# Performance work log

Hardware: AMD Instinct MI355X
Metric: run time of the kernel (lower is better)

## Reference

```python
import jax, jax.numpy as jnp
import numpy as np

EPS = 1e-5

def layer_norm(x, gamma):
    mu = jnp.mean(x, axis=-1, keepdims=True)
    var = jnp.mean(jnp.square(x - mu), axis=-1, keepdims=True)
    return (x - mu) / jnp.sqrt(var + EPS) * gamma

def setup_inputs() -> dict:
    key = jax.random.key(0)
    ks = jax.random.split(key, 10)
    b, n, j = 2, 2048, 2048
    dim, ctx_dim, heads, dim_head, ff_mult = 1024, 1024, 16, 64, 4
    inner = heads * dim_head
    ff_inner = ff_mult * dim
    s = 0.02
    return {
        'x': jax.random.normal(ks[0], (b, n, dim), jnp.float32),
        'context': jax.random.normal(ks[1], (b, j, ctx_dim), jnp.float32),
        'mask': jax.random.randint(ks[2], (b, j), 0, 2, jnp.int32),
        'gamma': jnp.ones((dim,), jnp.float32),
        'ctx_gamma': jnp.ones((ctx_dim,), jnp.float32),
        'Wq': jax.random.normal(ks[3], (dim, inner), jnp.float32) * s,
        'Wkv': jax.random.normal(ks[4], (ctx_dim, 2 * dim_head), jnp.float32) * s,
        'Wout': jax.random.normal(ks[5], (inner, dim), jnp.float32) * s,
        'Wff1': jax.random.normal(ks[6], (dim, 2 * ff_inner), jnp.float32) * s,
        'Wff2': jax.random.normal(ks[7], (ff_inner, dim), jnp.float32) * s,
    }

def reference(x, context, mask, gamma, ctx_gamma, Wq, Wkv, Wout, Wff1, Wff2):
    heads, dim_head = 16, 64
    b, n, dim = x.shape
    scale = dim_head ** -0.5
    xn = layer_norm(x, gamma)                              # [b,n,dim]
    ctx = layer_norm(context, ctx_gamma)                   # [b,j,cd]
    q = (xn @ Wq).reshape(b, n, heads, dim_head).transpose(0, 2, 1, 3) * scale  # [b,h,n,d]
    kv = ctx @ Wkv                                         # [b,j,2d]
    k, v = kv[..., :dim_head], kv[..., dim_head:]          # [b,j,d] each (multi-query)
    sim = jnp.einsum('bhid,bjd->bhij', q, k)               # [b,h,n,j]
    sim = jnp.where((mask == 0)[:, None, None, :], -jnp.inf, sim)
    attn = jax.nn.softmax(sim, axis=-1)
    out = jnp.einsum('bhij,bjd->bhid', attn, v)            # [b,h,n,d]
    out = out.transpose(0, 2, 1, 3).reshape(b, n, heads * dim_head)
    out = out @ Wout                                       # [b,n,dim]
    # parallel SwiGLU FF on normalized x
    h = xn @ Wff1
    ff_inner = Wff2.shape[0]
    a, gate = h[..., :ff_inner], h[..., ff_inner:]
    out = out + (jax.nn.silu(gate) * a) @ Wff2
    return out
```

## Files before the change

kernel.cpp:

```cpp
#include <hip/hip_runtime.h>

typedef unsigned short u16;
typedef unsigned int   u32;
typedef __bf16  bf16x8 __attribute__((ext_vector_type(8)));
typedef __bf16  bf16x2 __attribute__((ext_vector_type(2)));
typedef float   f32x4  __attribute__((ext_vector_type(4)));

static __device__ __forceinline__ float b2f(u16 v) {
    return __builtin_bit_cast(float, (u32)(((u32)v) << 16));
}
static __device__ __forceinline__ u16 f2b(float f) {
    u32 u = __builtin_bit_cast(u32, f);
    return (u16)((u + 0x7FFFu + ((u >> 16) & 1u)) >> 16);
}
static __device__ __forceinline__ u32 pack2(float a, float b) {
    bf16x2 t; t[0] = (__bf16)a; t[1] = (__bf16)b;
    return __builtin_bit_cast(u32, t);
}

__global__ __launch_bounds__(256)
void ln_kernel(const float* __restrict__ x, const float* __restrict__ ctx,
               const float* __restrict__ gamma, const float* __restrict__ cgamma,
               u16* __restrict__ xn, u16* __restrict__ ctxn)
{
    const int row = blockIdx.x;
    const int tid = threadIdx.x;
    const float* src; const float* g; u16* dst;
    if (row < 4096) { src = x   + (long)row * 1024;          g = gamma;  dst = xn   + (long)row * 1024; }
    else            { src = ctx + (long)(row - 4096) * 1024; g = cgamma; dst = ctxn + (long)(row - 4096) * 1024; }
    float4 v = ((const float4*)src)[tid];
    float s = v.x + v.y + v.z + v.w;
    float q = v.x*v.x + v.y*v.y + v.z*v.z + v.w*v.w;
#pragma unroll
    for (int off = 32; off; off >>= 1) { s += __shfl_xor(s, off); q += __shfl_xor(q, off); }
    __shared__ float r1[4], r2[4];
    if ((tid & 63) == 0) { r1[tid >> 6] = s; r2[tid >> 6] = q; }
    __syncthreads();
    s = r1[0] + r1[1] + r1[2] + r1[3];
    q = r2[0] + r2[1] + r2[2] + r2[3];
    float mu   = s * (1.0f / 1024.0f);
    float var  = q * (1.0f / 1024.0f) - mu * mu;
    float rstd = rsqrtf(var + 1e-5f);
    float4 gv = ((const float4*)g)[tid];
    ushort4 o;
    o.x = f2b((v.x - mu) * rstd * gv.x);
    o.y = f2b((v.y - mu) * rstd * gv.y);
    o.z = f2b((v.z - mu) * rstd * gv.z);
    o.w = f2b((v.w - mu) * rstd * gv.w);
    ((ushort4*)dst)[tid] = o;
}

__global__ __launch_bounds__(256)
void wconv(const float* __restrict__ W, u16* __restrict__ Wt, int N, int K, float scale)
{
    __shared__ float tile[32][33];
    const int tid = threadIdx.x;
    const int n0 = blockIdx.x * 32;
    const int k0 = blockIdx.y * 32;
    const int r  = tid >> 3;
    const int c4 = (tid & 7) * 4;
    float4 v = *(const float4*)&W[(long)(k0 + r) * N + n0 + c4];
    tile[r][c4 + 0] = v.x; tile[r][c4 + 1] = v.y; tile[r][c4 + 2] = v.z; tile[r][c4 + 3] = v.w;
    __syncthreads();
    ushort4 o;
    o.x = f2b(tile[c4 + 0][r] * scale);
    o.y = f2b(tile[c4 + 1][r] * scale);
    o.z = f2b(tile[c4 + 2][r] * scale);
    o.w = f2b(tile[c4 + 3][r] * scale);
    *(ushort4*)&Wt[(long)(n0 + r) * K + k0 + c4] = o;
}

__global__ __launch_bounds__(256)
void wconv_ff1(const float* __restrict__ W, u16* __restrict__ Wt)
{
    __shared__ float tile[32][33];
    const int tid = threadIdx.x;
    const int a  = blockIdx.x;
    const int k0 = blockIdx.y * 32;
    const int r  = tid >> 3;
    const int c4 = (tid & 7) * 4;
    const int srccol = (c4 < 16) ? (a * 16 + c4) : (4096 + a * 16 + (c4 - 16));
    float4 v = *(const float4*)&W[(long)(k0 + r) * 8192 + srccol];
    tile[r][c4 + 0] = v.x; tile[r][c4 + 1] = v.y; tile[r][c4 + 2] = v.z; tile[r][c4 + 3] = v.w;
    __syncthreads();
    ushort4 o;
    o.x = f2b(tile[c4 + 0][r]);
    o.y = f2b(tile[c4 + 1][r]);
    o.z = f2b(tile[c4 + 2][r]);
    o.w = f2b(tile[c4 + 3][r]);
    *(ushort4*)&Wt[(long)(a * 32 + r) * 1024 + k0 + c4] = o;
}

__global__ __launch_bounds__(256)
void kext_build(const float* __restrict__ kvf, const int* __restrict__ mask,
                u16* __restrict__ kext, float* __restrict__ mbias)
{
    const int gid = blockIdx.x * 256 + threadIdx.x;
    const int b = gid >> 14;
    const int rem = gid & 16383;
    const int j = rem >> 3;
    const int c = rem & 7;
    const float* src = &kvf[((long)b * 2048 + j) * 128 + c * 8];
    u16 ov[8];
#pragma unroll
    for (int e = 0; e < 8; ++e) ov[e] = f2b(src[e]);
    uint4 w;
    w.x = (u32)ov[0] | ((u32)ov[1] << 16);
    w.y = (u32)ov[2] | ((u32)ov[3] << 16);
    w.z = (u32)ov[4] | ((u32)ov[5] << 16);
    w.w = (u32)ov[6] | ((u32)ov[7] << 16);
    *(uint4*)&kext[((long)b * 2048 + j) * 64 + c * 8] = w;
    if (c == 0) mbias[b * 2048 + j] = mask[b * 2048 + j] ? 0.0f : -1e30f;
}

__global__ __launch_bounds__(256)
void vtrans(const float* __restrict__ kvf, u16* __restrict__ vT)
{
    const int j = blockIdx.x * 256 + threadIdx.x;
    const int d = blockIdx.y;
    const int b = blockIdx.z;
    vT[(long)b * 64 * 2048 + (long)d * 2048 + j] =
        f2b(kvf[((long)b * 2048 + j) * 128 + 64 + d]);
}

#define BM 128
#define BN 128
#define BK 32

template<int EPI>
__global__ __launch_bounds__(256, 2)
void gemm_bt(const u16* __restrict__ A, const u16* __restrict__ Bt,
             void* __restrict__ Cv,
             int K, int lda, int ldb, int ldc,
             long aH, long bH, long cH)
{
    __shared__ __align__(16) u16 sm[2][2][BM * BK];
    const int tid  = threadIdx.x;
    const int wave = tid >> 6;
    const int lane = tid & 63;
    const int tn = blockIdx.x * BN;
    const int tm = blockIdx.y * BM;
    const int z  = blockIdx.z;
    A  += (long)z * aH;
    Bt += (long)z * bH;

    const int arow0 = (tid >> 2);
    const int arow1 = 64 + (tid >> 2);
    const int acs0  = (tid & 3) ^ ((arow0 >> 1) & 3);
    const int acs1  = (tid & 3) ^ ((arow1 >> 1) & 3);
    const int nt = K / BK;

#define STAGE(buf, k0)                                                                              \
    do {                                                                                            \
        __builtin_amdgcn_global_load_lds(                                                           \
            (const __attribute__((address_space(1))) void*)(A + (long)(tm + arow0) * lda + (k0) + acs0 * 8),   \
            (__attribute__((address_space(3))) void*)(&sm[buf][0][(wave * 64) * 8]), 16, 0, 0);     \
        __builtin_amdgcn_global_load_lds(                                                           \
            (const __attribute__((address_space(1))) void*)(A + (long)(tm + arow1) * lda + (k0) + acs1 * 8),   \
            (__attribute__((address_space(3))) void*)(&sm[buf][0][(256 + wave * 64) * 8]), 16, 0, 0); \
        __builtin_amdgcn_global_load_lds(                                                           \
            (const __attribute__((address_space(1))) void*)(Bt + (long)(tn + arow0) * ldb + (k0) + acs0 * 8),  \
            (__attribute__((address_space(3))) void*)(&sm[buf][1][(wave * 64) * 8]), 16, 0, 0);     \
        __builtin_amdgcn_global_load_lds(                                                           \
            (const __attribute__((address_space(1))) void*)(Bt + (long)(tn + arow1) * ldb + (k0) + acs1 * 8),  \
            (__attribute__((address_space(3))) void*)(&sm[buf][1][(256 + wave * 64) * 8]), 16, 0, 0); \
    } while (0)

    STAGE(0, 0);

    f32x4 acc[4][4] = {};
    const int wr   = (wave >> 1) * 64;
    const int wc   = (wave & 1) * 64;
    const int frow = lane & 15;
    const int fk   = lane >> 4;

    for (int t = 0; t < nt; ++t) {
        __syncthreads();
        if (t + 1 < nt) STAGE((t + 1) & 1, (t + 1) * BK);
        const int cur = t & 1;
        bf16x8 af[4], bf[4];
#pragma unroll
        for (int m = 0; m < 4; ++m) {
            int row = wr + m * 16 + frow;
            af[m] = *(const bf16x8*)&sm[cur][0][row * BK + ((fk ^ ((row >> 1) & 3)) * 8)];
        }
#pragma unroll
        for (int n = 0; n < 4; ++n) {
            int row = wc + n * 16 + frow;
            bf[n] = *(const bf16x8*)&sm[cur][1][row * BK + ((fk ^ ((row >> 1) & 3)) * 8)];
        }
#pragma unroll
        for (int m = 0; m < 4; ++m)
#pragma unroll
            for (int n = 0; n < 4; ++n)
                acc[m][n] = __builtin_amdgcn_mfma_f32_16x16x32_bf16(af[m], bf[n], acc[m][n], 0, 0, 0);
    }
#undef STAGE

    const long coff = (long)z * cH;
#pragma unroll
    for (int m = 0; m < 4; ++m) {
        const int row0 = tm + wr + m * 16 + fk * 4;
#pragma unroll
        for (int n = 0; n < 4; ++n) {
            const int col = tn + wc + n * 16 + frow;
#pragma unroll
            for (int r = 0; r < 4; ++r) {
                const long off = coff + (long)(row0 + r) * ldc + col;
                const float v = acc[m][n][r];
                if constexpr (EPI == 0)      ((u16*)Cv)[off] = f2b(v);
                else if constexpr (EPI == 1) ((float*)Cv)[off] = v;
                else if constexpr (EPI == 2) ((float*)Cv)[off] += v;
                else                         atomicAdd(&((float*)Cv)[off], v);
            }
        }
    }
}

__global__ __launch_bounds__(512, 2)
void gemm256_ff1(const u16* __restrict__ A, const u16* __restrict__ Bt,
                 u16* __restrict__ C, int K, int lda, int ldb, int ldc)
{
    __shared__ __align__(16) u16 As[2][256 * 64];
    __shared__ __align__(16) u16 Bs[2][256 * 64];
    const int tid  = threadIdx.x;
    const int wave = tid >> 6, lane = tid & 63;
    const int wm = wave >> 2, wn = wave & 3;
    const int frow = lane & 15, fk = lane >> 4;
    const int tn = blockIdx.x * 256;
    const int tm = blockIdx.y * 256;
    const int nt = K >> 6;

    const int lrow  = lane >> 3;
    const int csrc8 = ((lane & 7) ^ lrow) * 8;
    int rbA0[2], rbA1[2], rbB0[2], rbB1[2];
#pragma unroll
    for (int g = 0; g < 2; ++g) {
        const int c = g * 8 + wave;
        const int a0 = ((c >> 3) * 128) + ((c & 7) * 8);
        rbA0[g] = a0; rbA1[g] = a0 + 64;
        const int b0 = ((c >> 2) * 64) + ((c & 3) * 8);
        rbB0[g] = b0; rbB1[g] = b0 + 32;
    }

#define STG(LDS, buf, src, toff, ld, kt, rb)                                                        \
    __builtin_amdgcn_global_load_lds(                                                               \
        (const __attribute__((address_space(1))) void*)((src) + (long)((toff) + (rb) + lrow) * (ld) + ((kt) << 6) + csrc8), \
        (__attribute__((address_space(3))) void*)(&LDS[buf][(rb) * 64]), 16, 0, 0)

#define STAGE_A0(buf, kt) do { STG(As, buf, A,  tm, lda, kt, rbA0[0]); STG(As, buf, A,  tm, lda, kt, rbA0[1]); } while (0)
#define STAGE_A1(buf, kt) do { STG(As, buf, A,  tm, lda, kt, rbA1[0]); STG(As, buf, A,  tm, lda, kt, rbA1[1]); } while (0)
#define STAGE_B0(buf, kt) do { STG(Bs, buf, Bt, tn, ldb, kt, rbB0[0]); STG(Bs, buf, Bt, tn, ldb, kt, rbB0[1]); } while (0)
#define STAGE_B1(buf, kt) do { STG(Bs, buf, Bt, tn, ldb, kt, rbB1[0]); STG(Bs, buf, Bt, tn, ldb, kt, rbB1[1]); } while (0)

    STAGE_B0(0, 0); STAGE_A0(0, 0); STAGE_A1(0, 0); STAGE_B1(0, 0);
    if (nt > 1) {
        STAGE_B0(1, 1); STAGE_A0(1, 1);
        asm volatile("s_waitcnt vmcnt(4)" ::: "memory");
    } else {
        asm volatile("s_waitcnt vmcnt(0)" ::: "memory");
    }
    __builtin_amdgcn_sched_barrier(0);
    __builtin_amdgcn_s_barrier();

    f32x4 acc[8][4] = {};

#define PHASE(mh, nh, STAGE_STMT)                                                                   \
    {                                                                                               \
        bf16x8 af[4][2], bfr[2][2];                                                                 \
        _Pragma("unroll") for (int i = 0; i < 4; ++i) {                                             \
            const int row = wm * 128 + (mh) * 64 + i * 16 + frow;                                   \
            _Pragma("unroll") for (int kk = 0; kk < 2; ++kk)                                        \
                af[i][kk] = *(const bf16x8*)&As[cur][row * 64 + (((kk * 4 + fk) ^ (row & 7)) * 8)]; \
        }                                                                                           \
        _Pragma("unroll") for (int j = 0; j < 2; ++j) {                                             \
            const int row = wn * 64 + (nh) * 32 + j * 16 + frow;                                    \
            _Pragma("unroll") for (int kk = 0; kk < 2; ++kk)                                        \
                bfr[j][kk] = *(const bf16x8*)&Bs[cur][row * 64 + (((kk * 4 + fk) ^ (row & 7)) * 8)];\
        }                                                                                           \
        STAGE_STMT;                                                                                 \
        __builtin_amdgcn_s_barrier();                                                               \
        asm volatile("s_waitcnt lgkmcnt(0)" ::: "memory");                                          \
        __builtin_amdgcn_sched_barrier(0);                                                          \
        __builtin_amdgcn_s_setprio(1);                                                              \
        _Pragma("unroll") for (int kk = 0; kk < 2; ++kk)                                            \
            _Pragma("unroll") for (int i = 0; i < 4; ++i)                                           \
                _Pragma("unroll") for (int j = 0; j < 2; ++j)                                       \
                    acc[(mh) * 4 + i][(nh) * 2 + j] = __builtin_amdgcn_mfma_f32_16x16x32_bf16(      \
                        af[i][kk], bfr[j][kk], acc[(mh) * 4 + i][(nh) * 2 + j], 0, 0, 0);           \
        __builtin_amdgcn_s_setprio(0);                                                              \
        __builtin_amdgcn_sched_barrier(0);                                                          \
    }

    for (int t = 0; t < nt; ++t) {
        const int cur = t & 1, nxt = cur ^ 1;
        PHASE(0, 0, if (t + 1 < nt) STAGE_A1(nxt, t + 1));
        __builtin_amdgcn_s_barrier();
        PHASE(1, 0, if (t + 1 < nt) STAGE_B1(nxt, t + 1));
        __builtin_amdgcn_s_barrier();
        PHASE(0, 1, if (t + 2 < nt) STAGE_B0(cur, t + 2));
        __builtin_amdgcn_s_barrier();
        PHASE(1, 1, if (t + 2 < nt) STAGE_A0(cur, t + 2));
        if (t + 1 < nt) {
            if (t + 2 < nt) asm volatile("s_waitcnt vmcnt(4)" ::: "memory");
            else            asm volatile("s_waitcnt vmcnt(0)" ::: "memory");
            __builtin_amdgcn_sched_barrier(0);
            __builtin_amdgcn_s_barrier();
        }
    }
#undef PHASE
#undef STAGE_A0
#undef STAGE_A1
#undef STAGE_B0
#undef STAGE_B1
#undef STG

#pragma unroll
    for (int mf = 0; mf < 8; ++mf) {
        const int gr = tm + wm * 128 + mf * 16 + fk * 4;
#pragma unroll
        for (int np = 0; np < 4; np += 2) {
            const int scol = (tn >> 1) + (wn * 2 + (np >> 1)) * 16 + frow;
            const f32x4 av = acc[mf][np];
            const f32x4 gv = acc[mf][np + 1];
#pragma unroll
            for (int r = 0; r < 4; ++r) {
                const float g = gv[r];
                const float o = av[r] * g / (1.0f + __expf(-g));
                C[(long)(gr + r) * ldc + scol] = f2b(o);
            }
        }
    }
}

__global__ __launch_bounds__(256, 4)
void flash_attn(const u16* __restrict__ qb, const u16* __restrict__ kext,
                const u16* __restrict__ vT, const float* __restrict__ mbias,
                u16* __restrict__ aout)
{
    __shared__ __align__(16) u16 Ksm[2][4096];
    __shared__ __align__(16) u16 Vsm[2][4096];
    __shared__ __align__(16) u16 Psm[4][1024];
    const int tid  = threadIdx.x;
    const int wave = tid >> 6, lane = tid & 63;
    const int frow = lane & 15, fk = lane >> 4;
    const int b = blockIdx.z, h = blockIdx.y;
    const int q0 = blockIdx.x * 64;

    const u16* kx = kext + (long)b * 2048 * 64;
    const u16* vb = vT   + (long)b * 64 * 2048;
    const float* mbb = mbias + b * 2048;

    const u16* qbase = qb + ((long)(b * 2048 + q0 + wave * 16 + frow)) * 1024 + h * 64;
    bf16x8 bq[2];
#pragma unroll
    for (int kk = 0; kk < 2; ++kk)
        bq[kk] = *(const bf16x8*)&qbase[kk * 32 + fk * 8];

#define FSTAGE(buf, j0s)                                                                             \
    do {                                                                                             \
        _Pragma("unroll")                                                                            \
        for (int i = 0; i < 2; ++i) {                                                                \
            const int slot = i * 256 + tid;                                                          \
            const int row  = slot >> 3;                                                              \
            const int csrc = (slot & 7) ^ (row & 7);                                                 \
            __builtin_amdgcn_global_load_lds(                                                        \
                (const __attribute__((address_space(1))) void*)(kx + (long)((j0s) + row) * 64 + csrc * 8), \
                (__attribute__((address_space(3))) void*)(&Ksm[buf][(i * 256 + wave * 64) * 8]), 16, 0, 0); \
            __builtin_amdgcn_global_load_lds(                                                        \
                (const __attribute__((address_space(1))) void*)(vb + (long)row * 2048 + (j0s) + csrc * 8),  \
                (__attribute__((address_space(3))) void*)(&Vsm[buf][(i * 256 + wave * 64) * 8]), 16, 0, 0); \
        }                                                                                            \
    } while (0)

    FSTAGE(0, 0);

    f32x4 oacc[4] = {};
    float mrun = -1e30f, lrun = 0.0f;
    u16* pw = &Psm[wave][0];

    for (int it = 0; it < 32; ++it) {
        const int j0 = it * 64;
        __syncthreads();
        float4 mb[4];
#pragma unroll
        for (int m = 0; m < 4; ++m)
            mb[m] = *(const float4*)&mbb[j0 + m * 16 + fk * 4];
        if (it + 1 < 32) FSTAGE((it + 1) & 1, (it + 1) * 64);
        const int cur = it & 1;

        f32x4 st[4] = {};
        __builtin_amdgcn_s_setprio(1);
#pragma unroll
        for (int kk = 0; kk < 2; ++kk) {
            bf16x8 ka[4];
#pragma unroll
            for (int m = 0; m < 4; ++m) {
                const int row = m * 16 + frow;
                ka[m] = *(const bf16x8*)&Ksm[cur][row * 64 + (((kk * 4 + fk) ^ (row & 7)) * 8)];
            }
#pragma unroll
            for (int m = 0; m < 4; ++m)
                st[m] = __builtin_amdgcn_mfma_f32_16x16x32_bf16(ka[m], bq[kk], st[m], 0, 0, 0);
        }
        __builtin_amdgcn_s_setprio(0);

        float sb[4][4];
#pragma unroll
        for (int m = 0; m < 4; ++m)
#pragma unroll
            for (int r = 0; r < 4; ++r) sb[m][r] = st[m][r] + (&mb[m].x)[r];
        float pm = fmaxf(
            fmaxf(fmaxf(sb[0][0], sb[0][1]), fmaxf(sb[0][2], sb[0][3])),
            fmaxf(fmaxf(sb[1][0], sb[1][1]), fmaxf(sb[1][2], sb[1][3])));
        pm = fmaxf(pm, fmaxf(
            fmaxf(fmaxf(sb[2][0], sb[2][1]), fmaxf(sb[2][2], sb[2][3])),
            fmaxf(fmaxf(sb[3][0], sb[3][1]), fmaxf(sb[3][2], sb[3][3]))));
        pm = fmaxf(pm, __shfl_xor(pm, 16));
        pm = fmaxf(pm, __shfl_xor(pm, 32));
        const float nm = fmaxf(mrun, pm);
        const float alpha = __expf(mrun - nm);
        mrun = nm;

        float rs = 0.0f;
#pragma unroll
        for (int m = 0; m < 4; ++m) {
            const float p0 = __expf(sb[m][0] - nm);
            const float p1 = __expf(sb[m][1] - nm);
            const float p2 = __expf(sb[m][2] - nm);
            const float p3 = __expf(sb[m][3] - nm);
            rs += (p0 + p1) + (p2 + p3);
            const int chunk = (m * 2 + (fk >> 1)) ^ (frow & 7);
            uint2 w; w.x = pack2(p0, p1); w.y = pack2(p2, p3);
            *(uint2*)&pw[frow * 64 + chunk * 8 + (fk & 1) * 4] = w;
        }
        rs += __shfl_xor(rs, 16);
        rs += __shfl_xor(rs, 32);
        lrun = lrun * alpha + rs;
#pragma unroll
        for (int mo = 0; mo < 4; ++mo)
#pragma unroll
            for (int r = 0; r < 4; ++r) oacc[mo][r] *= alpha;

        __builtin_amdgcn_s_setprio(1);
#pragma unroll
        for (int kkv = 0; kkv < 2; ++kkv) {
            bf16x8 va[4];
#pragma unroll
            for (int mo = 0; mo < 4; ++mo) {
                const int row = mo * 16 + frow;
                va[mo] = *(const bf16x8*)&Vsm[cur][row * 64 + (((kkv * 4 + fk) ^ (row & 7)) * 8)];
            }
            const bf16x8 pb = *(const bf16x8*)&pw[frow * 64 + (((kkv * 4 + fk) ^ (frow & 7)) * 8)];
#pragma unroll
            for (int mo = 0; mo < 4; ++mo)
                oacc[mo] = __builtin_amdgcn_mfma_f32_16x16x32_bf16(va[mo], pb, oacc[mo], 0, 0, 0);
        }
        __builtin_amdgcn_s_setprio(0);
    }
#undef FSTAGE

    const float inv = 1.0f / lrun;
    const long row = (long)b * 2048 + q0 + wave * 16 + frow;
#pragma unroll
    for (int mo = 0; mo < 4; ++mo) {
        uint2 w;
        w.x = pack2(oacc[mo][0] * inv, oacc[mo][1] * inv);
        w.y = pack2(oacc[mo][2] * inv, oacc[mo][3] * inv);
        *(uint2*)&aout[row * 1024 + h * 64 + mo * 16 + fk * 4] = w;
    }
}

extern "C" void kernel_launch(void* const* d_in, const int* in_sizes, int n_in,
                              void* d_out, int out_size, void* d_ws, size_t ws_size,
                              hipStream_t stream)
{
    const float* x      = (const float*)d_in[0];
    const float* ctx    = (const float*)d_in[1];
    const int*   mask   = (const int*)d_in[2];
    const float* gamma  = (const float*)d_in[3];
    const float* cgamma = (const float*)d_in[4];
    const float* Wq     = (const float*)d_in[5];
    const float* Wkv    = (const float*)d_in[6];
    const float* Wout   = (const float*)d_in[7];
    const float* Wff1   = (const float*)d_in[8];
    const float* Wff2   = (const float*)d_in[9];
    float* out = (float*)d_out;

    char* w = (char*)d_ws;
    auto carveB = [&](long bytes) { char* p = w; w += ((bytes + 255) / 256) * 256; return p; };
    u16*   xn     = (u16*)  carveB(4096L * 1024 * 2);
    u16*   ctxn   = (u16*)  carveB(4096L * 1024 * 2);
    u16*   WqT    = (u16*)  carveB(1024L * 1024 * 2);
    u16*   WkvT   = (u16*)  carveB(128L * 1024 * 2);
    u16*   WoutT  = (u16*)  carveB(1024L * 1024 * 2);
    u16*   Wff1Tp = (u16*)  carveB(8192L * 1024 * 2);
    u16*   Wff2T  = (u16*)  carveB(1024L * 4096 * 2);
    u16*   q      = (u16*)  carveB(4096L * 1024 * 2);
    float* kvf    = (float*)carveB(2L * 2048 * 128 * 4);
    u16*   kext   = (u16*)  carveB(2L * 2048 * 64 * 2);
    float* mbias  = (float*)carveB(2L * 2048 * 4);
    u16*   vT     = (u16*)  carveB(2L * 64 * 2048 * 2);
    u16*   aout   = (u16*)  carveB(4096L * 1024 * 2);
    u16*   gbuf   = (u16*)  carveB(4096L * 4096 * 2);

    dim3 B(256);

    ln_kernel<<<dim3(8192), B, 0, stream>>>(x, ctx, gamma, cgamma, xn, ctxn);
    wconv<<<dim3(32, 32),  B, 0, stream>>>(Wq,   WqT,   1024, 1024, 0.125f);
    wconv<<<dim3(4, 32),   B, 0, stream>>>(Wkv,  WkvT,  128,  1024, 1.0f);
    wconv<<<dim3(32, 32),  B, 0, stream>>>(Wout, WoutT, 1024, 1024, 1.0f);
    wconv_ff1<<<dim3(256, 32), B, 0, stream>>>(Wff1, Wff1Tp);
    wconv<<<dim3(32, 128), B, 0, stream>>>(Wff2, Wff2T, 1024, 4096, 1.0f);

    gemm_bt<0><<<dim3(8, 32, 1), B, 0, stream>>>(xn, WqT, q, 1024, 1024, 1024, 1024, 0, 0, 0);
    hipMemsetAsync(kvf, 0, 2L * 2048 * 128 * 4, stream);
    gemm_bt<4><<<dim3(1, 32, 4), B, 0, stream>>>(ctxn, WkvT, kvf, 256, 1024, 1024, 128, 256, 256, 0);
    kext_build<<<dim3(128), B, 0, stream>>>(kvf, mask, kext, mbias);
    vtrans<<<dim3(8, 64, 2), B, 0, stream>>>(kvf, vT);

    flash_attn<<<dim3(32, 16, 2), B, 0, stream>>>(q, kext, vT, mbias, aout);

    gemm_bt<1><<<dim3(8, 32, 1), B, 0, stream>>>(aout, WoutT, out, 1024, 1024, 1024, 1024, 0, 0, 0);
    gemm256_ff1<<<dim3(32, 16), dim3(512), 0, stream>>>(xn, Wff1Tp, gbuf, 1024, 1024, 1024, 4096);
    gemm_bt<4><<<dim3(8, 32, 2), B, 0, stream>>>(gbuf, Wff2T, out, 2048, 4096, 4096, 1024, 2048, 2048, 0);
}
```

Baseline: 418.7 us.

## Generalize 256-tile GEMM, reorder fragment reuse, and use it for FF2 split-K

Turns the 256x256 FF1 GEMM into a templated kernel with a batch/split-K offset and an atomic-add epilogue, then uses it for the FF2 projection with 4-way split-K instead of the smaller-tile gemm_bt. The inner loop is also reordered so A and B fragments read from LDS are reused across quadrants (snake order), which cuts LDS reads per K-step. The aim is higher arithmetic intensity and fewer LDS reads for the largest GEMM. In exchange it holds more fragment registers and does more fp32 atomics, since split-K goes from 2 to 4.

```diff
diff --git a/kernel.cpp b/kernel.cpp
--- a/kernel.cpp
+++ b/kernel.cpp
@@ -217,9 +217,11 @@
     }
 }
 
+template<int EPI>
 __global__ __launch_bounds__(512, 2)
-void gemm256_ff1(const u16* __restrict__ A, const u16* __restrict__ Bt,
-                 u16* __restrict__ C, int K, int lda, int ldb, int ldc)
+void gemm256(const u16* __restrict__ A, const u16* __restrict__ Bt,
+             void* __restrict__ Cv, int K, int lda, int ldb, int ldc,
+             long aH, long bH)
 {
     __shared__ __align__(16) u16 As[2][256 * 64];
     __shared__ __align__(16) u16 Bs[2][256 * 64];
@@ -229,6 +231,9 @@
     const int frow = lane & 15, fk = lane >> 4;
     const int tn = blockIdx.x * 256;
     const int tm = blockIdx.y * 256;
+    const int z  = blockIdx.z;
+    A  += (long)z * aH;
+    Bt += (long)z * bH;
     const int nt = K >> 6;
 
     const int lrow  = lane >> 3;
@@ -253,6 +258,30 @@
 #define STAGE_B0(buf, kt) do { STG(Bs, buf, Bt, tn, ldb, kt, rbB0[0]); STG(Bs, buf, Bt, tn, ldb, kt, rbB0[1]); } while (0)
 #define STAGE_B1(buf, kt) do { STG(Bs, buf, Bt, tn, ldb, kt, rbB1[0]); STG(Bs, buf, Bt, tn, ldb, kt, rbB1[1]); } while (0)
 
+#define DSREAD_A(dst, half)                                                                         \
+    do { _Pragma("unroll") for (int i = 0; i < 4; ++i) {                                            \
+        const int row = wm * 128 + (half) * 64 + i * 16 + frow;                                     \
+        _Pragma("unroll") for (int kk = 0; kk < 2; ++kk)                                            \
+            dst[i][kk] = *(const bf16x8*)&As[cur][row * 64 + (((kk * 4 + fk) ^ (row & 7)) * 8)];    \
+    } } while (0)
+#define DSREAD_B(dst, half)                                                                         \
+    do { _Pragma("unroll") for (int j = 0; j < 2; ++j) {                                            \
+        const int row = wn * 64 + (half) * 32 + j * 16 + frow;                                      \
+        _Pragma("unroll") for (int kk = 0; kk < 2; ++kk)                                            \
+            dst[j][kk] = *(const bf16x8*)&Bs[cur][row * 64 + (((kk * 4 + fk) ^ (row & 7)) * 8)];    \
+    } } while (0)
+#define MFMA_Q(afr, bfr, mh, nh)                                                                    \
+    do { __builtin_amdgcn_s_setprio(1);                                                             \
+    _Pragma("unroll") for (int kk = 0; kk < 2; ++kk)                                                \
+        _Pragma("unroll") for (int i = 0; i < 4; ++i)                                               \
+            _Pragma("unroll") for (int j = 0; j < 2; ++j)                                           \
+                acc[(mh) * 4 + i][(nh) * 2 + j] = __builtin_amdgcn_mfma_f32_16x16x32_bf16(          \
+                    afr[i][kk], bfr[j][kk], acc[(mh) * 4 + i][(nh) * 2 + j], 0, 0, 0);              \
+    __builtin_amdgcn_s_setprio(0); } while (0)
+#define LGKM0 do { asm volatile("s_waitcnt lgkmcnt(0)" ::: "memory"); __builtin_amdgcn_sched_barrier(0); } while (0)
+#define SB    __builtin_amdgcn_sched_barrier(0)
+#define BAR   __builtin_amdgcn_s_barrier()
+
     STAGE_B0(0, 0); STAGE_A0(0, 0); STAGE_A1(0, 0); STAGE_B1(0, 0);
     if (nt > 1) {
         STAGE_B0(1, 1); STAGE_A0(1, 1);
@@ -260,74 +289,81 @@
     } else {
         asm volatile("s_waitcnt vmcnt(0)" ::: "memory");
     }
-    __builtin_amdgcn_sched_barrier(0);
-    __builtin_amdgcn_s_barrier();
+    SB;
+    BAR;
 
     f32x4 acc[8][4] = {};
-
-#define PHASE(mh, nh, STAGE_STMT)                                                                   \
-    {                                                                                               \
-        bf16x8 af[4][2], bfr[2][2];                                                                 \
-        _Pragma("unroll") for (int i = 0; i < 4; ++i) {                                             \
-            const int row = wm * 128 + (mh) * 64 + i * 16 + frow;                                   \
-            _Pragma("unroll") for (int kk = 0; kk < 2; ++kk)                                        \
-                af[i][kk] = *(const bf16x8*)&As[cur][row * 64 + (((kk * 4 + fk) ^ (row & 7)) * 8)]; \
-        }                                                                                           \
-        _Pragma("unroll") for (int j = 0; j < 2; ++j) {                                             \
-            const int row = wn * 64 + (nh) * 32 + j * 16 + frow;                                    \
-            _Pragma("unroll") for (int kk = 0; kk < 2; ++kk)                                        \
-                bfr[j][kk] = *(const bf16x8*)&Bs[cur][row * 64 + (((kk * 4 + fk) ^ (row & 7)) * 8)];\
-        }                                                                                           \
-        STAGE_STMT;                                                                                 \
-        __builtin_amdgcn_s_barrier();                                                               \
-        asm volatile("s_waitcnt lgkmcnt(0)" ::: "memory");                                          \
-        __builtin_amdgcn_sched_barrier(0);                                                          \
-        __builtin_amdgcn_s_setprio(1);                                                              \
-        _Pragma("unroll") for (int kk = 0; kk < 2; ++kk)                                            \
-            _Pragma("unroll") for (int i = 0; i < 4; ++i)                                           \
-                _Pragma("unroll") for (int j = 0; j < 2; ++j)                                       \
-                    acc[(mh) * 4 + i][(nh) * 2 + j] = __builtin_amdgcn_mfma_f32_16x16x32_bf16(      \
-                        af[i][kk], bfr[j][kk], acc[(mh) * 4 + i][(nh) * 2 + j], 0, 0, 0);           \
-        __builtin_amdgcn_s_setprio(0);                                                              \
-        __builtin_amdgcn_sched_barrier(0);                                                          \
-    }
+    bf16x8 a0f[4][2], a1f[4][2], b0f[2][2], b1f[2][2];
 
     for (int t = 0; t < nt; ++t) {
         const int cur = t & 1, nxt = cur ^ 1;
-        PHASE(0, 0, if (t + 1 < nt) STAGE_A1(nxt, t + 1));
-        __builtin_amdgcn_s_barrier();
-        PHASE(1, 0, if (t + 1 < nt) STAGE_B1(nxt, t + 1));
-        __builtin_amdgcn_s_barrier();
-        PHASE(0, 1, if (t + 2 < nt) STAGE_B0(cur, t + 2));
-        __builtin_amdgcn_s_barrier();
-        PHASE(1, 1, if (t + 2 < nt) STAGE_A0(cur, t + 2));
+        DSREAD_A(a0f, 0); DSREAD_B(b0f, 0);
+        if (t + 1 < nt) STAGE_A1(nxt, t + 1);
+        BAR; LGKM0;
+        MFMA_Q(a0f, b0f, 0, 0);
+        SB; BAR;
+        DSREAD_B(b1f, 1);
+        if (t + 1 < nt) STAGE_B1(nxt, t + 1);
+        BAR; LGKM0;
+        MFMA_Q(a0f, b1f, 0, 1);
+        SB; BAR;
+        DSREAD_A(a1f, 1);
+        if (t + 2 < nt) STAGE_B0(cur, t + 2);
+        BAR; LGKM0;
+        MFMA_Q(a1f, b1f, 1, 1);
+        SB; BAR;
+        if (t + 2 < nt) STAGE_A0(cur, t + 2);
+        BAR;
+        MFMA_Q(a1f, b0f, 1, 0);
+        SB;
         if (t + 1 < nt) {
             if (t + 2 < nt) asm volatile("s_waitcnt vmcnt(4)" ::: "memory");
             else            asm volatile("s_waitcnt vmcnt(0)" ::: "memory");
-            __builtin_amdgcn_sched_barrier(0);
-            __builtin_amdgcn_s_barrier();
-        }
-    }
-#undef PHASE
+            SB;
+            BAR;
+        }
+    }
+#undef BAR
+#undef SB
+#undef LGKM0
+#undef MFMA_Q
+#undef DSREAD_A
+#undef DSREAD_B
 #undef STAGE_A0
 #undef STAGE_A1
 #undef STAGE_B0
 #undef STAGE_B1
 #undef STG
 
-#pragma unroll
-    for (int mf = 0; mf < 8; ++mf) {
-        const int gr = tm + wm * 128 + mf * 16 + fk * 4;
-#pragma unroll
-        for (int np = 0; np < 4; np += 2) {
-            const int scol = (tn >> 1) + (wn * 2 + (np >> 1)) * 16 + frow;
-            const f32x4 av = acc[mf][np];
-            const f32x4 gv = acc[mf][np + 1];
-#pragma unroll
-            for (int r = 0; r < 4; ++r) {
-                const float g = gv[r];
-                const float o = av[r] * g / (1.0f + __expf(-g));
-                C[(long)(gr + r) * ldc + scol] = f2b(o);
+    if constexpr (EPI == 3) {
+        u16* C = (u16*)Cv;
+#pragma unroll
+        for (int mf = 0; mf < 8; ++mf) {
+            const int gr = tm + wm * 128 + mf * 16 + fk * 4;
+#pragma unroll
+            for (int np = 0; np < 4; np += 2) {
+                const int scol = (tn >> 1) + (wn * 2 + (np >> 1)) * 16 + frow;
+                const f32x4 av = acc[mf][np];
+                const f32x4 gv = acc[mf][np + 1];
+#pragma unroll
+                for (int r = 0; r < 4; ++r) {
+                    const float g = gv[r];
+                    const float o = av[r] * g / (1.0f + __expf(-g));
+                    C[(long)(gr + r) * ldc + scol] = f2b(o);
+                }
+            }
+        }
+    } else {
+        float* C = (float*)Cv;
+#pragma unroll
+        for (int mf = 0; mf < 8; ++mf) {
+            const int gr = tm + wm * 128 + mf * 16 + fk * 4;
+#pragma unroll
+            for (int nf = 0; nf < 4; ++nf) {
+                const int col = tn + wn * 64 + nf * 16 + frow;
+#pragma unroll
+                for (int r = 0; r < 4; ++r)
+                    atomicAdd(&C[(long)(gr + r) * ldc + col], acc[mf][nf][r]);
             }
         }
     }
@@ -522,6 +558,6 @@
     flash_attn<<<dim3(32, 16, 2), B, 0, stream>>>(q, kext, vT, mbias, aout);
 
     gemm_bt<1><<<dim3(8, 32, 1), B, 0, stream>>>(aout, WoutT, out, 1024, 1024, 1024, 1024, 0, 0, 0);
-    gemm256_ff1<<<dim3(32, 16), dim3(512), 0, stream>>>(xn, Wff1Tp, gbuf, 1024, 1024, 1024, 4096);
-    gemm_bt<4><<<dim3(8, 32, 2), B, 0, stream>>>(gbuf, Wff2T, out, 2048, 4096, 4096, 1024, 2048, 2048, 0);
-}
+    gemm256<3><<<dim3(32, 16, 1), dim3(512), 0, stream>>>(xn, Wff1Tp, gbuf, 1024, 1024, 1024, 4096, 0, 0);
+    gemm256<4><<<dim3(4, 16, 4), dim3(512), 0, stream>>>(gbuf, Wff2T, out, 1024, 4096, 4096, 1024, 1024, 1024);
+}
```

After: 423.2 us. About the same (+1.1%).
